# Kernel optimization log

Hardware: AMD Instinct MI355X
Metric: run time of the kernel (lower is better)

## Reference

```python
import jax, jax.numpy as jnp
import numpy as np

EMBED_DIM = 1024
NUM_HEADS = 16
HEAD_DIM = EMBED_DIM // NUM_HEADS
FF_DIM = 4 * EMBED_DIM
LN_EPS = 1e-5


def _layernorm(x, g, b):
    mu = jnp.mean(x, axis=-1, keepdims=True)
    var = jnp.var(x, axis=-1, keepdims=True)
    return (x - mu) * jax.lax.rsqrt(var + LN_EPS) * g + b


def setup_inputs() -> dict:
    key = jax.random.key(0)
    ks = jax.random.split(key, 8)
    B, T, C = 2, 2048, EMBED_DIM
    s_c = 1.0 / np.sqrt(C)
    s_f = 1.0 / np.sqrt(FF_DIM)
    return {
        "x": jax.random.normal(ks[0], (B, T, C), jnp.float32),
        "ln1_g": jnp.ones((C,), jnp.float32),
        "ln1_b": jnp.zeros((C,), jnp.float32),
        "qkv_w": jax.random.uniform(ks[1], (C, 3 * C), jnp.float32, -s_c, s_c),
        "qkv_b": jnp.zeros((3 * C,), jnp.float32),
        "out_w": jax.random.uniform(ks[2], (C, C), jnp.float32, -s_c, s_c),
        "out_b": jnp.zeros((C,), jnp.float32),
        "ln2_g": jnp.ones((C,), jnp.float32),
        "ln2_b": jnp.zeros((C,), jnp.float32),
        "ff1_w": jax.random.uniform(ks[3], (C, FF_DIM), jnp.float32, -s_c, s_c),
        "ff1_b": jnp.zeros((FF_DIM,), jnp.float32),
        "ff2_w": jax.random.uniform(ks[4], (FF_DIM, C), jnp.float32, -s_f, s_f),
        "ff2_b": jnp.zeros((C,), jnp.float32),
    }


def reference(x, ln1_g, ln1_b, qkv_w, qkv_b, out_w, out_b,
              ln2_g, ln2_b, ff1_w, ff1_b, ff2_w, ff2_b):
    B, T, C = x.shape
    H, D = NUM_HEADS, HEAD_DIM

    # --- pre-LN causal self-attention ---
    h = _layernorm(x, ln1_g, ln1_b)
    qkv = h @ qkv_w + qkv_b                      # [B,T,3C]
    q, k, v = jnp.split(qkv, 3, axis=-1)
    q = q.reshape(B, T, H, D)
    k = k.reshape(B, T, H, D)
    v = v.reshape(B, T, H, D)
    scores = jnp.einsum('bqhd,bkhd->bhqk', q, k) / np.sqrt(D)  # [B,H,T,T]
    causal = jnp.tril(jnp.ones((T, T), bool))
    scores = jnp.where(causal, scores, -jnp.inf)
    attn = jax.nn.softmax(scores, axis=-1)
    o = jnp.einsum('bhqk,bkhd->bqhd', attn, v).reshape(B, T, C)
    x = x + o @ out_w + out_b

    # --- GELU MLP ---
    h2 = _layernorm(x, ln2_g, ln2_b)
    ff = jax.nn.gelu(h2 @ ff1_w + ff1_b, approximate=False) @ ff2_w + ff2_b
    return x + ff
```

## Files before the change

### kernel.cpp

```cpp
#include <hip/hip_runtime.h>
#include <hip/hip_bf16.h>
#include <math.h>

#define B_ 2
#define T_ 2048
#define C_ 1024
#define H_ 16
#define D_ 64
#define F_ 4096
#define BT_ (B_*T_)

typedef __attribute__((ext_vector_type(8))) short bf16x8;
typedef __attribute__((ext_vector_type(4))) float f32x4;

__device__ __forceinline__ float bfraw2f(unsigned int u){
    union { unsigned int i; float f; } c; c.i = u << 16; return c.f;
}
__device__ __forceinline__ short f2bfraw(float f){
    union { float f; unsigned int i; } c; c.f = f;
    unsigned int u = c.i;
    u += 0x7fffu + ((u >> 16) & 1u);
    return (short)(u >> 16);
}
__device__ __forceinline__ void gl2lds16(const void* g, void* l) {
    __builtin_amdgcn_global_load_lds(
        (const __attribute__((address_space(1))) unsigned int*)g,
        (__attribute__((address_space(3))) unsigned int*)l,
        16, 0, 0);
}

__global__ __launch_bounds__(256) void wconv_t(const float* __restrict__ W,
                                               short* __restrict__ Wt,
                                               int K, int N)
{
    __shared__ short tile[64][65];
    int k0 = blockIdx.y * 64, n0 = blockIdx.x * 64;
    int t = threadIdx.x;
#pragma unroll
    for (int i = 0; i < 4; i++) {
        int idx = t + i * 256;
        int r = idx >> 4, c4 = (idx & 15) * 4;
        float4 u = *(const float4*)(W + (size_t)(k0 + r) * N + n0 + c4);
        tile[c4 + 0][r] = f2bfraw(u.x);
        tile[c4 + 1][r] = f2bfraw(u.y);
        tile[c4 + 2][r] = f2bfraw(u.z);
        tile[c4 + 3][r] = f2bfraw(u.w);
    }
    __syncthreads();
#pragma unroll
    for (int i = 0; i < 2; i++) {
        int idx = t + i * 256;
        int r = idx >> 3, c8 = (idx & 7) * 8;
        short v[8];
#pragma unroll
        for (int u8 = 0; u8 < 8; u8++) v[u8] = tile[r][c8 + u8];
        *(uint4*)(Wt + (size_t)(n0 + r) * K + k0 + c8) = *(const uint4*)v;
    }
}

__global__ __launch_bounds__(256) void v_transpose(const __hip_bfloat16* __restrict__ qkv,
                                                   short* __restrict__ vt)
{
    __shared__ short tile[64][65];
    int kb = blockIdx.x * 64;
    int h = blockIdx.y, b = blockIdx.z;
    const short* src = (const short*)qkv + (size_t)b * T_ * 3 * C_ + 2 * C_ + h * D_;
    int t = threadIdx.x;
#pragma unroll
    for (int i = 0; i < 2; i++) {
        int idx = t + i * 256;
        int r = idx >> 3, c8 = (idx & 7) * 8;
        bf16x8 v = *(const bf16x8*)(src + (size_t)(kb + r) * 3 * C_ + c8);
#pragma unroll
        for (int u = 0; u < 8; u++) tile[c8 + u][r] = v[u];
    }
    __syncthreads();
    short* dst = vt + (size_t)(b * H_ + h) * D_ * T_ + kb;
#pragma unroll
    for (int i = 0; i < 2; i++) {
        int idx = t + i * 256;
        int r = idx >> 3, c8 = (idx & 7) * 8;
        short v[8];
#pragma unroll
        for (int u = 0; u < 8; u++) v[u] = tile[r][c8 + u];
        *(uint4*)(dst + (size_t)r * T_ + c8) = *(const uint4*)v;
    }
}

__global__ __launch_bounds__(256) void ln_fused(const float* __restrict__ x, int ldx,
                                                const float* __restrict__ g,
                                                const float* __restrict__ b,
                                                __hip_bfloat16* out, int ldo)
{
    __shared__ float sm1[4], sm2[4];
    __shared__ float smu, srs;
    int row = blockIdx.x, t = threadIdx.x;
    const float* xr = x + (size_t)row * ldx;
    float v[4]; float s = 0.f, ss = 0.f;
#pragma unroll
    for (int i = 0; i < 4; i++) {
        float f = xr[t + i * 256];
        v[i] = f; s += f; ss += f * f;
    }
#pragma unroll
    for (int off = 32; off >= 1; off >>= 1) {
        s  += __shfl_xor(s,  off);
        ss += __shfl_xor(ss, off);
    }
    int wave = t >> 6, lane = t & 63;
    if (!lane) { sm1[wave] = s; sm2[wave] = ss; }
    __syncthreads();
    if (t == 0) {
        s  = sm1[0] + sm1[1] + sm1[2] + sm1[3];
        ss = sm2[0] + sm2[1] + sm2[2] + sm2[3];
        float mu  = s * (1.f / C_);
        float var = ss * (1.f / C_) - mu * mu;
        if (var < 0.f) var = 0.f;
        smu = mu; srs = rsqrtf(var + 1e-5f);
    }
    __syncthreads();
    float mu = smu, rs = srs;
#pragma unroll
    for (int i = 0; i < 4; i++) {
        int c = t + i * 256;
        out[(size_t)row * ldo + c] = __float2bfloat16((v[i] - mu) * rs * g[c] + b[c]);
    }
}

template<int ACT>
__global__ __launch_bounds__(256) void gemm128(
    const __hip_bfloat16* A, int lda,
    const short* Wt, int ldw, int noff, int koff,
    const float* __restrict__ bias, int boff,
    void* out, int ldo,
    int K)
{
    __shared__ __align__(16) short As[3][128 * 32];
    __shared__ __align__(16) short Bs[3][128 * 32];
    int tid = threadIdx.x;
    int w = tid >> 6, lane = tid & 63;
    int quad = lane >> 4, l16 = lane & 15;
    int wm = w >> 1, wn = w & 1;
    int m0 = blockIdx.y * 128, n0 = blockIdx.x * 128;
    int lr = lane >> 2, lk = (lane & 3) * 8;

    const __hip_bfloat16* Ag = A + (size_t)(m0 + w * 32 + lr) * lda + lk;
    const short*          Bg = Wt + (size_t)(noff + n0 + w * 32 + lr) * ldw + koff + lk;

    f32x4 acc[4][4];
#pragma unroll
    for (int i = 0; i < 4; i++)
#pragma unroll
        for (int j = 0; j < 4; j++) acc[i][j] = (f32x4){0.f, 0.f, 0.f, 0.f};

    const int NT = K >> 5;
    {
        gl2lds16(Ag,            &As[0][(w * 32) * 32]);
        gl2lds16(Ag + 16 * lda, &As[0][(w * 32 + 16) * 32]);
        gl2lds16(Bg,            &Bs[0][(w * 32) * 32]);
        gl2lds16(Bg + 16 * ldw, &Bs[0][(w * 32 + 16) * 32]);
        if (NT > 1) {
            gl2lds16(Ag + 32,            &As[1][(w * 32) * 32]);
            gl2lds16(Ag + 16 * lda + 32, &As[1][(w * 32 + 16) * 32]);
            gl2lds16(Bg + 32,            &Bs[1][(w * 32) * 32]);
            gl2lds16(Bg + 16 * ldw + 32, &Bs[1][(w * 32 + 16) * 32]);
        }
    }

    int cur = 0;
    for (int t = 0; t < NT; t++) {
        if (t + 2 < NT) {
            int sb = cur + 2; if (sb >= 3) sb -= 3;
            int ko = (t + 2) << 5;
            gl2lds16(Ag + ko,            &As[sb][(w * 32) * 32]);
            gl2lds16(Ag + 16 * lda + ko, &As[sb][(w * 32 + 16) * 32]);
            gl2lds16(Bg + ko,            &Bs[sb][(w * 32) * 32]);
            gl2lds16(Bg + 16 * ldw + ko, &Bs[sb][(w * 32 + 16) * 32]);
        }
        int ahead = NT - 1 - t;
        if (ahead >= 2)      asm volatile("s_waitcnt vmcnt(8)" ::: "memory");
        else if (ahead == 1) asm volatile("s_waitcnt vmcnt(4)" ::: "memory");
        else                 asm volatile("s_waitcnt vmcnt(0)" ::: "memory");
        __builtin_amdgcn_s_barrier();
        __builtin_amdgcn_sched_barrier(0);

        bf16x8 af[4], bfr[4];
#pragma unroll
        for (int mt = 0; mt < 4; mt++)
            af[mt] = *(const bf16x8*)&As[cur][(wm * 64 + mt * 16 + l16) * 32 + quad * 8];
#pragma unroll
        for (int nt = 0; nt < 4; nt++)
            bfr[nt] = *(const bf16x8*)&Bs[cur][(wn * 64 + nt * 16 + l16) * 32 + quad * 8];
#pragma unroll
        for (int mt = 0; mt < 4; mt++)
#pragma unroll
            for (int nt = 0; nt < 4; nt++)
                acc[mt][nt] = __builtin_amdgcn_mfma_f32_16x16x32_bf16(af[mt], bfr[nt], acc[mt][nt], 0, 0, 0);

        __builtin_amdgcn_sched_barrier(0);
        __builtin_amdgcn_s_barrier();
        cur = (cur == 2) ? 0 : cur + 1;
    }

#pragma unroll
    for (int nt = 0; nt < 4; nt++) {
        int c = n0 + wn * 64 + nt * 16 + l16;
        float bv = bias ? bias[boff + c] : 0.f;
#pragma unroll
        for (int mt = 0; mt < 4; mt++) {
#pragma unroll
            for (int reg = 0; reg < 4; reg++) {
                int r = m0 + wm * 64 + mt * 16 + quad * 4 + reg;
                float v = acc[mt][nt][reg] + bv;
                if (ACT == 1) v = 0.5f * v * (1.f + erff(v * 0.70710678118654752f));
                ((__hip_bfloat16*)out)[(size_t)r * ldo + c] = __float2bfloat16(v);
            }
        }
    }
}

__global__ __launch_bounds__(256) void gemm64n(
    const __hip_bfloat16* A, int lda,
    const short* Wt, int ldw, int koff,
    const float* __restrict__ bias,
    const float* res, int ldres,
    float* out, int ldo,
    int K)
{
    __shared__ __align__(16) short As[3][128 * 32];
    __shared__ __align__(16) short Bs[3][64 * 32];
    int tid = threadIdx.x;
    int w = tid >> 6, lane = tid & 63;
    int quad = lane >> 4, l16 = lane & 15;
    int wm = w >> 1, wn = w & 1;
    int m0 = blockIdx.y * 128, n0 = blockIdx.x * 64;
    int lr = lane >> 2, lk = (lane & 3) * 8;

    const __hip_bfloat16* Ag = A + (size_t)(m0 + w * 32 + lr) * lda + lk;
    const short*          Bg = Wt + (size_t)(n0 + w * 16 + lr) * ldw + koff + lk;

    f32x4 acc[4][2];
#pragma unroll
    for (int i = 0; i < 4; i++)
#pragma unroll
        for (int j = 0; j < 2; j++) acc[i][j] = (f32x4){0.f, 0.f, 0.f, 0.f};

    const int NT = K >> 5;
    {
        gl2lds16(Ag,            &As[0][(w * 32) * 32]);
        gl2lds16(Ag + 16 * lda, &As[0][(w * 32 + 16) * 32]);
        gl2lds16(Bg,            &Bs[0][(w * 16) * 32]);
        if (NT > 1) {
            gl2lds16(Ag + 32,            &As[1][(w * 32) * 32]);
            gl2lds16(Ag + 16 * lda + 32, &As[1][(w * 32 + 16) * 32]);
            gl2lds16(Bg + 32,            &Bs[1][(w * 16) * 32]);
        }
    }

    int cur = 0;
    for (int t = 0; t < NT; t++) {
        if (t + 2 < NT) {
            int sb = cur + 2; if (sb >= 3) sb -= 3;
            int ko = (t + 2) << 5;
            gl2lds16(Ag + ko,            &As[sb][(w * 32) * 32]);
            gl2lds16(Ag + 16 * lda + ko, &As[sb][(w * 32 + 16) * 32]);
            gl2lds16(Bg + ko,            &Bs[sb][(w * 16) * 32]);
        }
        int ahead = NT - 1 - t;
        if (ahead >= 2)      asm volatile("s_waitcnt vmcnt(6)" ::: "memory");
        else if (ahead == 1) asm volatile("s_waitcnt vmcnt(3)" ::: "memory");
        else                 asm volatile("s_waitcnt vmcnt(0)" ::: "memory");
        __builtin_amdgcn_s_barrier();
        __builtin_amdgcn_sched_barrier(0);

        bf16x8 af[4], bfr[2];
#pragma unroll
        for (int mt = 0; mt < 4; mt++)
            af[mt] = *(const bf16x8*)&As[cur][(wm * 64 + mt * 16 + l16) * 32 + quad * 8];
#pragma unroll
        for (int nt = 0; nt < 2; nt++)
            bfr[nt] = *(const bf16x8*)&Bs[cur][(wn * 32 + nt * 16 + l16) * 32 + quad * 8];
#pragma unroll
        for (int mt = 0; mt < 4; mt++)
#pragma unroll
            for (int nt = 0; nt < 2; nt++)
                acc[mt][nt] = __builtin_amdgcn_mfma_f32_16x16x32_bf16(af[mt], bfr[nt], acc[mt][nt], 0, 0, 0);

        __builtin_amdgcn_sched_barrier(0);
        __builtin_amdgcn_s_barrier();
        cur = (cur == 2) ? 0 : cur + 1;
    }

#pragma unroll
    for (int nt = 0; nt < 2; nt++) {
        int c = n0 + wn * 32 + nt * 16 + l16;
        float bv = bias ? bias[c] : 0.f;
#pragma unroll
        for (int mt = 0; mt < 4; mt++) {
#pragma unroll
            for (int reg = 0; reg < 4; reg++) {
                int r = m0 + wm * 64 + mt * 16 + quad * 4 + reg;
                float v = acc[mt][nt][reg] + bv + res[(size_t)r * ldres + c];
                out[(size_t)r * ldo + c] = v;
            }
        }
    }
}

__global__ __launch_bounds__(256, 2) void attn_flash(__hip_bfloat16* qkv,
                                                     const short* __restrict__ vt)
{
    __shared__ __align__(16) short Ks[2][64 * 64];
    __shared__ __align__(16) short Vs[2][64 * 64];
    __shared__ __align__(16) short Pl[4][16 * 72];
    int tid = threadIdx.x;
    int wave = tid >> 6, lane = tid & 63;
    int quad = lane >> 4, l16 = lane & 15;
    int fid = blockIdx.x + 16 * blockIdx.y;
    int h = (fid & 7) * 2 + ((fid >> 3) >> 4);
    int i = (fid >> 3) & 15;
    int b = blockIdx.z;
    int qbs[2]; qbs[0] = i; qbs[1] = 31 - i;
    const size_t rs = 3 * C_;
    __hip_bfloat16* base = qkv + (size_t)b * T_ * rs;
    const __hip_bfloat16* Qb = base + h * D_;
    const __hip_bfloat16* Kb = base + C_ + h * D_;
    const short* Vt = vt + (size_t)(b * H_ + h) * D_ * T_;

    bf16x8 qf[2][2];
#pragma unroll
    for (int tq = 0; tq < 2; tq++) {
        const __hip_bfloat16* qr = Qb + (size_t)(qbs[tq] * 64 + wave * 16 + l16) * rs + quad * 8;
        qf[tq][0] = *(const bf16x8*)qr;
        qf[tq][1] = *(const bf16x8*)(qr + 32);
    }

    f32x4 o[2][4];
    float m[2][4], l[2][4];
#pragma unroll
    for (int tq = 0; tq < 2; tq++)
#pragma unroll
        for (int t = 0; t < 4; t++) {
            o[tq][t] = (f32x4){0.f, 0.f, 0.f, 0.f};
            m[tq][t] = -INFINITY;
            l[tq][t] = 0.f;
        }
    short* Pw = &Pl[wave][0];

    int srow = wave * 16 + (lane >> 3);
    int scg  = ((lane & 7) ^ (lane >> 3)) * 8;
    const __hip_bfloat16* Kg = Kb + (size_t)srow * rs + scg;
    const short*          Vg = Vt + (size_t)srow * T_ + scg;

    int cur = 0;
#pragma unroll
    for (int j = 0; j < 2; j++) {
        gl2lds16(Kg + (size_t)(j * 8) * rs, &Ks[0][(wave * 2 + j) * 512]);
        gl2lds16(Vg + (size_t)(j * 8) * T_, &Vs[0][(wave * 2 + j) * 512]);
    }
    __syncthreads();

    int qhi = qbs[1];
    int swz = (l16 & 7);
    for (int kt = 0; kt <= qhi; kt++) {
        if (kt < qhi) {
            int kb = (kt + 1) * 64;
#pragma unroll
            for (int j = 0; j < 2; j++) {
                gl2lds16(Kg + (size_t)(kb + j * 8) * rs, &Ks[cur ^ 1][(wave * 2 + j) * 512]);
                gl2lds16(Vg + (size_t)(j * 8) * T_ + kb, &Vs[cur ^ 1][(wave * 2 + j) * 512]);
            }
        }
        const short* Kc = Ks[cur];
        const short* Vc = Vs[cur];
#pragma unroll
        for (int tq = 0; tq < 2; tq++) {
            if (tq == 0 && kt > qbs[0]) continue;
            f32x4 sa[4];
            __builtin_amdgcn_s_setprio(1);
#pragma unroll
            for (int t16 = 0; t16 < 4; t16++) {
                int row = t16 * 16 + l16;
                bf16x8 kf0 = *(const bf16x8*)&Kc[row * 64 + ((quad     ^ swz)) * 8];
                bf16x8 kf1 = *(const bf16x8*)&Kc[row * 64 + (((quad + 4) ^ swz)) * 8];
                f32x4 s = (f32x4){0.f, 0.f, 0.f, 0.f};
                s = __builtin_amdgcn_mfma_f32_16x16x32_bf16(qf[tq][0], kf0, s, 0, 0, 0);
                s = __builtin_amdgcn_mfma_f32_16x16x32_bf16(qf[tq][1], kf1, s, 0, 0, 0);
                sa[t16] = s;
            }
            __builtin_amdgcn_s_setprio(0);
            bool maskit = (kt == qbs[tq]);
#pragma unroll
            for (int t16 = 0; t16 < 4; t16++) {
#pragma unroll
                for (int reg = 0; reg < 4; reg++) {
                    float v = sa[t16][reg] * 0.125f;
                    if (maskit) {
                        int keyl = t16 * 16 + l16;
                        int ql = wave * 16 + quad * 4 + reg;
                        if (keyl > ql) v = -3.0e38f;
                    }
                    sa[t16][reg] = v;
                }
            }
            float mx[4];
#pragma unroll
            for (int reg = 0; reg < 4; reg++)
                mx[reg] = fmaxf(fmaxf(sa[0][reg], sa[1][reg]), fmaxf(sa[2][reg], sa[3][reg]));
#pragma unroll
            for (int off = 8; off >= 1; off >>= 1)
#pragma unroll
                for (int reg = 0; reg < 4; reg++)
                    mx[reg] = fmaxf(mx[reg], __shfl_xor(mx[reg], off));
            float alpha[4];
#pragma unroll
            for (int reg = 0; reg < 4; reg++) {
                float mn = fmaxf(m[tq][reg], mx[reg]);
                alpha[reg] = __expf(m[tq][reg] - mn);
                m[tq][reg] = mn;
            }
            float rsum[4] = {0.f, 0.f, 0.f, 0.f};
#pragma unroll
            for (int t16 = 0; t16 < 4; t16++) {
#pragma unroll
                for (int reg = 0; reg < 4; reg++) {
                    float p = __expf(sa[t16][reg] - m[tq][reg]);
                    rsum[reg] += p;
                    Pw[(quad * 4 + reg) * 72 + t16 * 16 + l16] = f2bfraw(p);
                }
            }
#pragma unroll
            for (int off = 8; off >= 1; off >>= 1)
#pragma unroll
                for (int reg = 0; reg < 4; reg++)
                    rsum[reg] += __shfl_xor(rsum[reg], off);
#pragma unroll
            for (int reg = 0; reg < 4; reg++)
                l[tq][reg] = l[tq][reg] * alpha[reg] + rsum[reg];
#pragma unroll
            for (int t = 0; t < 4; t++)
#pragma unroll
                for (int reg = 0; reg < 4; reg++)
                    o[tq][t][reg] *= alpha[reg];
            __builtin_amdgcn_s_setprio(1);
#pragma unroll
            for (int chunk = 0; chunk < 2; chunk++) {
                bf16x8 pf = *(const bf16x8*)&Pw[l16 * 72 + chunk * 32 + quad * 8];
#pragma unroll
                for (int dt = 0; dt < 4; dt++) {
                    int row = dt * 16 + l16;
                    bf16x8 vf = *(const bf16x8*)&Vc[row * 64 + (((chunk * 4 + quad) ^ swz)) * 8];
                    o[tq][dt] = __builtin_amdgcn_mfma_f32_16x16x32_bf16(pf, vf, o[tq][dt], 0, 0, 0);
                }
            }
            __builtin_amdgcn_s_setprio(0);
        }
        __syncthreads();
        cur ^= 1;
    }

#pragma unroll
    for (int tq = 0; tq < 2; tq++) {
#pragma unroll
        for (int dt = 0; dt < 4; dt++) {
#pragma unroll
            for (int reg = 0; reg < 4; reg++) {
                int r = qbs[tq] * 64 + wave * 16 + quad * 4 + reg;
                float v = o[tq][dt][reg] / l[tq][reg];
                base[(size_t)r * rs + h * D_ + dt * 16 + l16] = __float2bfloat16(v);
            }
        }
    }
}

extern "C" void kernel_launch(void* const* d_in, const int* in_sizes, int n_in,
                              void* d_out, int out_size, void* d_ws, size_t ws_size,
                              hipStream_t stream)
{
    const float* x     = (const float*)d_in[0];
    const float* ln1_g = (const float*)d_in[1];
    const float* ln1_b = (const float*)d_in[2];
    const float* qkv_w = (const float*)d_in[3];
    const float* qkv_b = (const float*)d_in[4];
    const float* out_w = (const float*)d_in[5];
    const float* out_b = (const float*)d_in[6];
    const float* ln2_g = (const float*)d_in[7];
    const float* ln2_b = (const float*)d_in[8];
    const float* ff1_w = (const float*)d_in[9];
    const float* ff1_b = (const float*)d_in[10];
    const float* ff2_w = (const float*)d_in[11];
    const float* ff2_b = (const float*)d_in[12];

    char* ws = (char*)d_ws;
    __hip_bfloat16* qkv = (__hip_bfloat16*)ws;
    short* qkvwT = (short*)(ws + 25165824);
    short* outwT = (short*)(ws + 31457280);
    short* ff1wT = (short*)(ws + 33554432);
    short* ff2wT = (short*)(ws + 41943040);
    __hip_bfloat16* hbuf2 = qkv;
    __hip_bfloat16* act   = qkv + 1024;
    __hip_bfloat16* hbuf1 = (__hip_bfloat16*)d_out;
    float* x1 = (float*)d_out;
    short* vtbuf = (short*)d_out;

    wconv_t<<<dim3(3 * C_ / 64, C_ / 64), 256, 0, stream>>>(qkv_w, qkvwT, C_, 3 * C_);
    wconv_t<<<dim3(C_ / 64, C_ / 64),     256, 0, stream>>>(out_w, outwT, C_, C_);
    wconv_t<<<dim3(F_ / 64, C_ / 64),     256, 0, stream>>>(ff1_w, ff1wT, C_, F_);
    wconv_t<<<dim3(C_ / 64, F_ / 64),     256, 0, stream>>>(ff2_w, ff2wT, F_, C_);

    ln_fused<<<BT_, 256, 0, stream>>>(x, C_, ln1_g, ln1_b, hbuf1, C_);
    gemm128<0><<<dim3(3 * C_ / 128, BT_ / 128), 256, 0, stream>>>(
        hbuf1, C_, qkvwT, C_, 0, 0, qkv_b, 0, qkv, 3 * C_, C_);
    v_transpose<<<dim3(T_ / 64, H_, B_), 256, 0, stream>>>(qkv, vtbuf);
    attn_flash<<<dim3(16, H_, B_), 256, 0, stream>>>(qkv, vtbuf);
    gemm64n<<<dim3(C_ / 64, BT_ / 128), 256, 0, stream>>>(
        qkv, 3 * C_, outwT, C_, 0, out_b, x, C_, x1, C_, C_);
    ln_fused<<<BT_, 256, 0, stream>>>(x1, C_, ln2_g, ln2_b, hbuf2, 3 * C_);
    for (int f = 0; f < 2; f++) {
        gemm128<1><<<dim3(2048 / 128, BT_ / 128), 256, 0, stream>>>(
            hbuf2, 3 * C_, ff1wT, C_, f * 2048, 0, ff1_b, f * 2048,
            act, 3 * C_, C_);
        gemm64n<<<dim3(C_ / 64, BT_ / 128), 256, 0, stream>>>(
            act, 3 * C_, ff2wT, F_, f * 2048, (f == 0 ? ff2_b : nullptr),
            x1, C_, x1, C_, 2048);
    }
}
```

Baseline: 431.5 us.

## Merge weight conversions into one launch and process two KV tiles per barrier

Replaces the four weight-transpose/convert launches with a single kernel that maps a flat block index onto each weight matrix, which saves three launches. In attention, each pipeline stage now stages two 64-key K/V tiles (128 keys) in a double buffer, so the number of __syncthreads and prefetch rounds is halved. The cost is doubled LDS use for K/V (64 KB vs 32 KB per block), which may cut occupancy under launch_bounds(256,2). It also wastes some loads when the last stage holds only one valid tile.

```diff
diff --git a/kernel.cpp b/kernel.cpp
--- a/kernel.cpp
+++ b/kernel.cpp
@@ -29,12 +29,21 @@
         16, 0, 0);
 }
 
-__global__ __launch_bounds__(256) void wconv_t(const float* __restrict__ W,
-                                               short* __restrict__ Wt,
-                                               int K, int N)
-{
+__global__ __launch_bounds__(256) void wconv_all(const float* qkv_w, short* qkvwT,
+                                                 const float* out_w, short* outwT,
+                                                 const float* ff1_w, short* ff1wT,
+                                                 const float* ff2_w, short* ff2wT)
+{
+    int id = blockIdx.x;
+    const float* W; short* Wt; int K, N;
+    if (id < 768)       { W = qkv_w; Wt = qkvwT; K = C_; N = 3 * C_; }
+    else if (id < 1024) { id -= 768;  W = out_w; Wt = outwT; K = C_; N = C_; }
+    else if (id < 2048) { id -= 1024; W = ff1_w; Wt = ff1wT; K = C_; N = F_; }
+    else                { id -= 2048; W = ff2_w; Wt = ff2wT; K = F_; N = C_; }
+    int ntile = N >> 6;
+    int n0 = (id % ntile) * 64, k0 = (id / ntile) * 64;
+
     __shared__ short tile[64][65];
-    int k0 = blockIdx.y * 64, n0 = blockIdx.x * 64;
     int t = threadIdx.x;
 #pragma unroll
     for (int i = 0; i < 4; i++) {
@@ -310,8 +319,8 @@
 __global__ __launch_bounds__(256, 2) void attn_flash(__hip_bfloat16* qkv,
                                                      const short* __restrict__ vt)
 {
-    __shared__ __align__(16) short Ks[2][64 * 64];
-    __shared__ __align__(16) short Vs[2][64 * 64];
+    __shared__ __align__(16) short Ks[2][2][64 * 64];
+    __shared__ __align__(16) short Vs[2][2][64 * 64];
     __shared__ __align__(16) short Pl[4][16 * 72];
     int tid = threadIdx.x;
     int wave = tid >> 6, lane = tid & 63;
@@ -352,108 +361,119 @@
     const __hip_bfloat16* Kg = Kb + (size_t)srow * rs + scg;
     const short*          Vg = Vt + (size_t)srow * T_ + scg;
 
+    int qhi = qbs[1];
+    int NS = (qhi >> 1) + 1;
+    int swz = (l16 & 7);
     int cur = 0;
-#pragma unroll
-    for (int j = 0; j < 2; j++) {
-        gl2lds16(Kg + (size_t)(j * 8) * rs, &Ks[0][(wave * 2 + j) * 512]);
-        gl2lds16(Vg + (size_t)(j * 8) * T_, &Vs[0][(wave * 2 + j) * 512]);
-    }
+
+#pragma unroll
+    for (int sub = 0; sub < 2; sub++)
+#pragma unroll
+        for (int j = 0; j < 2; j++) {
+            gl2lds16(Kg + (size_t)(sub * 64 + j * 8) * rs, &Ks[0][sub][(wave * 2 + j) * 512]);
+            gl2lds16(Vg + (size_t)(j * 8) * T_ + sub * 64, &Vs[0][sub][(wave * 2 + j) * 512]);
+        }
     __syncthreads();
 
-    int qhi = qbs[1];
-    int swz = (l16 & 7);
-    for (int kt = 0; kt <= qhi; kt++) {
-        if (kt < qhi) {
-            int kb = (kt + 1) * 64;
-#pragma unroll
-            for (int j = 0; j < 2; j++) {
-                gl2lds16(Kg + (size_t)(kb + j * 8) * rs, &Ks[cur ^ 1][(wave * 2 + j) * 512]);
-                gl2lds16(Vg + (size_t)(j * 8) * T_ + kb, &Vs[cur ^ 1][(wave * 2 + j) * 512]);
+    for (int s = 0; s < NS; s++) {
+        if (s + 1 < NS) {
+            int kb = (s + 1) * 128;
+#pragma unroll
+            for (int sub = 0; sub < 2; sub++)
+#pragma unroll
+                for (int j = 0; j < 2; j++) {
+                    gl2lds16(Kg + (size_t)(kb + sub * 64 + j * 8) * rs, &Ks[cur ^ 1][sub][(wave * 2 + j) * 512]);
+                    gl2lds16(Vg + (size_t)(j * 8) * T_ + kb + sub * 64, &Vs[cur ^ 1][sub][(wave * 2 + j) * 512]);
+                }
+        }
+#pragma unroll
+        for (int sub = 0; sub < 2; sub++) {
+            int kt = 2 * s + sub;
+            if (kt > qhi) break;
+            const short* Kc = Ks[cur][sub];
+            const short* Vc = Vs[cur][sub];
+#pragma unroll
+            for (int tq = 0; tq < 2; tq++) {
+                if (kt > qbs[tq]) continue;
+                f32x4 sa[4];
+                __builtin_amdgcn_s_setprio(1);
+#pragma unroll
+                for (int t16 = 0; t16 < 4; t16++) {
+                    int row = t16 * 16 + l16;
+                    bf16x8 kf0 = *(const bf16x8*)&Kc[row * 64 + ((quad     ^ swz)) * 8];
+                    bf16x8 kf1 = *(const bf16x8*)&Kc[row * 64 + (((quad + 4) ^ swz)) * 8];
+                    f32x4 sv = (f32x4){0.f, 0.f, 0.f, 0.f};
+                    sv = __builtin_amdgcn_mfma_f32_16x16x32_bf16(qf[tq][0], kf0, sv, 0, 0, 0);
+                    sv = __builtin_amdgcn_mfma_f32_16x16x32_bf16(qf[tq][1], kf1, sv, 0, 0, 0);
+                    sa[t16] = sv;
+                }
+                __builtin_amdgcn_s_setprio(0);
+                bool maskit = (kt == qbs[tq]);
+#pragma unroll
+                for (int t16 = 0; t16 < 4; t16++) {
+#pragma unroll
+                    for (int reg = 0; reg < 4; reg++) {
+                        float v = sa[t16][reg] * 0.125f;
+                        if (maskit) {
+                            int keyl = t16 * 16 + l16;
+                            int ql = wave * 16 + quad * 4 + reg;
+                            if (keyl > ql) v = -3.0e38f;
+                        }
+                        sa[t16][reg] = v;
+                    }
+                }
+                float mx[4];
+#pragma unroll
+                for (int reg = 0; reg < 4; reg++)
+                    mx[reg] = fmaxf(fmaxf(sa[0][reg], sa[1][reg]), fmaxf(sa[2][reg], sa[3][reg]));
+#pragma unroll
+                for (int off = 8; off >= 1; off >>= 1)
+#pragma unroll
+                    for (int reg = 0; reg < 4; reg++)
+                        mx[reg] = fmaxf(mx[reg], __shfl_xor(mx[reg], off));
+                float alpha[4];
+#pragma unroll
+                for (int reg = 0; reg < 4; reg++) {
+                    float mn = fmaxf(m[tq][reg], mx[reg]);
+                    alpha[reg] = __expf(m[tq][reg] - mn);
+                    m[tq][reg] = mn;
+                }
+                float rsum[4] = {0.f, 0.f, 0.f, 0.f};
+#pragma unroll
+                for (int t16 = 0; t16 < 4; t16++) {
+#pragma unroll
+                    for (int reg = 0; reg < 4; reg++) {
+                        float p = __expf(sa[t16][reg] - m[tq][reg]);
+                        rsum[reg] += p;
+                        Pw[(quad * 4 + reg) * 72 + t16 * 16 + l16] = f2bfraw(p);
+                    }
+                }
+#pragma unroll
+                for (int off = 8; off >= 1; off >>= 1)
+#pragma unroll
+                    for (int reg = 0; reg < 4; reg++)
+                        rsum[reg] += __shfl_xor(rsum[reg], off);
+#pragma unroll
+                for (int reg = 0; reg < 4; reg++)
+                    l[tq][reg] = l[tq][reg] * alpha[reg] + rsum[reg];
+#pragma unroll
+                for (int t = 0; t < 4; t++)
+#pragma unroll
+                    for (int reg = 0; reg < 4; reg++)
+                        o[tq][t][reg] *= alpha[reg];
+                __builtin_amdgcn_s_setprio(1);
+#pragma unroll
+                for (int chunk = 0; chunk < 2; chunk++) {
+                    bf16x8 pf = *(const bf16x8*)&Pw[l16 * 72 + chunk * 32 + quad * 8];
+#pragma unroll
+                    for (int dt = 0; dt < 4; dt++) {
+                        int row = dt * 16 + l16;
+                        bf16x8 vf = *(const bf16x8*)&Vc[row * 64 + (((chunk * 4 + quad) ^ swz)) * 8];
+                        o[tq][dt] = __builtin_amdgcn_mfma_f32_16x16x32_bf16(pf, vf, o[tq][dt], 0, 0, 0);
+                    }
+                }
+                __builtin_amdgcn_s_setprio(0);
             }
-        }
-        const short* Kc = Ks[cur];
-        const short* Vc = Vs[cur];
-#pragma unroll
-        for (int tq = 0; tq < 2; tq++) {
-            if (tq == 0 && kt > qbs[0]) continue;
-            f32x4 sa[4];
-            __builtin_amdgcn_s_setprio(1);
-#pragma unroll
-            for (int t16 = 0; t16 < 4; t16++) {
-                int row = t16 * 16 + l16;
-                bf16x8 kf0 = *(const bf16x8*)&Kc[row * 64 + ((quad     ^ swz)) * 8];
-                bf16x8 kf1 = *(const bf16x8*)&Kc[row * 64 + (((quad + 4) ^ swz)) * 8];
-                f32x4 s = (f32x4){0.f, 0.f, 0.f, 0.f};
-                s = __builtin_amdgcn_mfma_f32_16x16x32_bf16(qf[tq][0], kf0, s, 0, 0, 0);
-                s = __builtin_amdgcn_mfma_f32_16x16x32_bf16(qf[tq][1], kf1, s, 0, 0, 0);
-                sa[t16] = s;
-            }
-            __builtin_amdgcn_s_setprio(0);
-            bool maskit = (kt == qbs[tq]);
-#pragma unroll
-            for (int t16 = 0; t16 < 4; t16++) {
-#pragma unroll
-                for (int reg = 0; reg < 4; reg++) {
-                    float v = sa[t16][reg] * 0.125f;
-                    if (maskit) {
-                        int keyl = t16 * 16 + l16;
-                        int ql = wave * 16 + quad * 4 + reg;
-                        if (keyl > ql) v = -3.0e38f;
-                    }
-                    sa[t16][reg] = v;
-                }
-            }
-            float mx[4];
-#pragma unroll
-            for (int reg = 0; reg < 4; reg++)
-                mx[reg] = fmaxf(fmaxf(sa[0][reg], sa[1][reg]), fmaxf(sa[2][reg], sa[3][reg]));
-#pragma unroll
-            for (int off = 8; off >= 1; off >>= 1)
-#pragma unroll
-                for (int reg = 0; reg < 4; reg++)
-                    mx[reg] = fmaxf(mx[reg], __shfl_xor(mx[reg], off));
-            float alpha[4];
-#pragma unroll
-            for (int reg = 0; reg < 4; reg++) {
-                float mn = fmaxf(m[tq][reg], mx[reg]);
-                alpha[reg] = __expf(m[tq][reg] - mn);
-                m[tq][reg] = mn;
-            }
-            float rsum[4] = {0.f, 0.f, 0.f, 0.f};
-#pragma unroll
-            for (int t16 = 0; t16 < 4; t16++) {
-#pragma unroll
-                for (int reg = 0; reg < 4; reg++) {
-                    float p = __expf(sa[t16][reg] - m[tq][reg]);
-                    rsum[reg] += p;
-                    Pw[(quad * 4 + reg) * 72 + t16 * 16 + l16] = f2bfraw(p);
-                }
-            }
-#pragma unroll
-            for (int off = 8; off >= 1; off >>= 1)
-#pragma unroll
-                for (int reg = 0; reg < 4; reg++)
-                    rsum[reg] += __shfl_xor(rsum[reg], off);
-#pragma unroll
-            for (int reg = 0; reg < 4; reg++)
-                l[tq][reg] = l[tq][reg] * alpha[reg] + rsum[reg];
-#pragma unroll
-            for (int t = 0; t < 4; t++)
-#pragma unroll
-                for (int reg = 0; reg < 4; reg++)
-                    o[tq][t][reg] *= alpha[reg];
-            __builtin_amdgcn_s_setprio(1);
-#pragma unroll
-            for (int chunk = 0; chunk < 2; chunk++) {
-                bf16x8 pf = *(const bf16x8*)&Pw[l16 * 72 + chunk * 32 + quad * 8];
-#pragma unroll
-                for (int dt = 0; dt < 4; dt++) {
-                    int row = dt * 16 + l16;
-                    bf16x8 vf = *(const bf16x8*)&Vc[row * 64 + (((chunk * 4 + quad) ^ swz)) * 8];
-                    o[tq][dt] = __builtin_amdgcn_mfma_f32_16x16x32_bf16(pf, vf, o[tq][dt], 0, 0, 0);
-                }
-            }
-            __builtin_amdgcn_s_setprio(0);
         }
         __syncthreads();
         cur ^= 1;
@@ -503,10 +523,8 @@
     float* x1 = (float*)d_out;
     short* vtbuf = (short*)d_out;
 
-    wconv_t<<<dim3(3 * C_ / 64, C_ / 64), 256, 0, stream>>>(qkv_w, qkvwT, C_, 3 * C_);
-    wconv_t<<<dim3(C_ / 64, C_ / 64),     256, 0, stream>>>(out_w, outwT, C_, C_);
-    wconv_t<<<dim3(F_ / 64, C_ / 64),     256, 0, stream>>>(ff1_w, ff1wT, C_, F_);
-    wconv_t<<<dim3(C_ / 64, F_ / 64),     256, 0, stream>>>(ff2_w, ff2wT, F_, C_);
+    wconv_all<<<3072, 256, 0, stream>>>(qkv_w, qkvwT, out_w, outwT,
+                                        ff1_w, ff1wT, ff2_w, ff2wT);
 
     ln_fused<<<BT_, 256, 0, stream>>>(x, C_, ln1_g, ln1_b, hbuf1, C_);
     gemm128<0><<<dim3(3 * C_ / 128, BT_ / 128), 256, 0, stream>>>(
```

After: 425.4 us. About the same (-1.4%).
